# Kernel optimization log

Measured on AMD Instinct MI355X. Metric: run time of the kernel, lower is better.

## Reference

```python
import jax, jax.numpy as jnp
import numpy as np

EPS = 1e-5  # torch LayerNorm default
NUM_HEADS = 12


def layer_norm(x, g, b):
    m = jnp.mean(x, axis=-1, keepdims=True)
    v = jnp.var(x, axis=-1, keepdims=True)
    return (x - m) * jax.lax.rsqrt(v + EPS) * g + b


def split_heads(x):
    B, N, C = x.shape
    return x.reshape(B, N, NUM_HEADS, C // NUM_HEADS).transpose(0, 2, 1, 3)  # [B,H,N,D]


def merge_heads(x):
    B, H, N, D = x.shape
    return x.transpose(0, 2, 1, 3).reshape(B, N, H * D)


def attn_core(q, k, v, mask):
    # q:[B,H,Nq,D], k/v:[B,H,Nk,D], mask:[B,Nk] float (1=keep)
    d = q.shape[-1]
    scores = jnp.einsum('bhqd,bhkd->bhqk', q, k) * (d ** -0.5)
    scores = scores + (1.0 - mask)[:, None, None, :] * -5.0
    a = jax.nn.softmax(scores, axis=-1)
    return jnp.einsum('bhqk,bhkd->bhqd', a, v)


def setup_inputs() -> dict:
    key = jax.random.key(0)
    B, N, C = 4, 1024, 768
    Hd = C * 4  # mlp hidden = 3072
    ks = jax.random.split(key, 12)
    s = 0.02
    inp = {
        'x': jax.random.normal(ks[0], (B, N, C), jnp.float32),
        'encoder_out': jax.random.normal(ks[1], (B, N, C), jnp.float32),
        'mask': jnp.ones((B, N), jnp.float32),
        'encoder_mask': jnp.ones((B, N), jnp.float32),
        'ln1_g': jnp.ones((C,), jnp.float32), 'ln1_b': jnp.zeros((C,), jnp.float32),
        'qkv_w': jax.random.normal(ks[2], (C, 3 * C), jnp.float32) * s,
        'sa_proj_w': jax.random.normal(ks[3], (C, C), jnp.float32) * s,
        'sa_proj_b': jnp.zeros((C,), jnp.float32),
        'ln2_g': jnp.ones((C,), jnp.float32), 'ln2_b': jnp.zeros((C,), jnp.float32),
        'q_w': jax.random.normal(ks[4], (C, C), jnp.float32) * s,
        'kv_w': jax.random.normal(ks[5], (C, 2 * C), jnp.float32) * s,
        'ca_proj_w': jax.random.normal(ks[6], (C, C), jnp.float32) * s,
        'ca_proj_b': jnp.zeros((C,), jnp.float32),
        'ln3_g': jnp.ones((C,), jnp.float32), 'ln3_b': jnp.zeros((C,), jnp.float32),
        'fc1_w': jax.random.normal(ks[7], (C, Hd), jnp.float32) * s,
        'fc1_b': jnp.zeros((Hd,), jnp.float32),
        'fc2_w': jax.random.normal(ks[8], (Hd, C), jnp.float32) * s,
        'fc2_b': jnp.zeros((C,), jnp.float32),
    }
    return inp


def reference(x, encoder_out, mask, encoder_mask,
              ln1_g, ln1_b, qkv_w, sa_proj_w, sa_proj_b,
              ln2_g, ln2_b, q_w, kv_w, ca_proj_w, ca_proj_b,
              ln3_g, ln3_b, fc1_w, fc1_b, fc2_w, fc2_b):
    B, N, C = x.shape
    D = C // NUM_HEADS
    # --- self attention ---
    h = layer_norm(x, ln1_g, ln1_b)
    qkv = (h @ qkv_w).reshape(B, N, 3, NUM_HEADS, D)
    q = qkv[:, :, 0].transpose(0, 2, 1, 3)
    k = qkv[:, :, 1].transpose(0, 2, 1, 3)
    v = qkv[:, :, 2].transpose(0, 2, 1, 3)
    o = merge_heads(attn_core(q, k, v, mask)) @ sa_proj_w + sa_proj_b
    x = x + o
    # --- cross attention ---
    h = layer_norm(x, ln2_g, ln2_b)
    q = split_heads(h @ q_w)
    Be, Ne, Ce = encoder_out.shape
    kv = (encoder_out @ kv_w).reshape(Be, Ne, 2, NUM_HEADS, D)
    k = kv[:, :, 0].transpose(0, 2, 1, 3)
    v = kv[:, :, 1].transpose(0, 2, 1, 3)
    o = merge_heads(attn_core(q, k, v, encoder_mask)) @ ca_proj_w + ca_proj_b
    x = x + o
    # --- MLP (exact GELU, like torch nn.GELU default) ---
    h = layer_norm(x, ln3_g, ln3_b)
    h = jax.nn.gelu(h @ fc1_w + fc1_b, approximate=False) @ fc2_w + fc2_b
    return x + h
```

## Files before the change

kernel.cpp:

```cpp
#include <hip/hip_runtime.h>

typedef __attribute__((ext_vector_type(8))) __bf16 bf16x8;
typedef __attribute__((ext_vector_type(4))) float f32x4;

__device__ __forceinline__ void gload_lds16(const __bf16* g, __bf16* l) {
    __builtin_amdgcn_global_load_lds(
        (const __attribute__((address_space(1))) void*)g,
        (__attribute__((address_space(3))) void*)l,
        16, 0, 0);
}

template <int N> struct WaitVm;
#define WV(n) template <> struct WaitVm<n> { static __device__ __forceinline__ void run() { \
    asm volatile("s_waitcnt vmcnt(" #n ")" ::: "memory"); } };
WV(0) WV(3) WV(4) WV(6) WV(8) WV(9) WV(12)
#undef WV

__global__ void transpose_f2b(const float* __restrict__ in, __bf16* __restrict__ outp,
                              int R, int Ccols) {
    __shared__ __bf16 tile[32][33];
    int bx = blockIdx.x * 32, by = blockIdx.y * 32;
    int tx = threadIdx.x & 31, ty = threadIdx.x >> 5;
#pragma unroll
    for (int i = ty; i < 32; i += 8)
        tile[i][tx] = (__bf16)in[(size_t)(by + i) * Ccols + bx + tx];
    __syncthreads();
#pragma unroll
    for (int i = ty; i < 32; i += 8)
        outp[(size_t)(bx + i) * R + by + tx] = tile[tx][i];
}

__global__ void cvt_f2b(const float* __restrict__ in, __bf16* __restrict__ outp) {
    int i = blockIdx.x * blockDim.x + threadIdx.x;
    float4 v = ((const float4*)in)[i];
    __bf16 o4[4] = {(__bf16)v.x, (__bf16)v.y, (__bf16)v.z, (__bf16)v.w};
    *(uint2*)(outp + (size_t)i * 4) = *(const uint2*)o4;
}

__global__ __launch_bounds__(256) void ln_kernel(const float* __restrict__ x,
                                                 const float* __restrict__ g,
                                                 const float* __restrict__ b,
                                                 __bf16* __restrict__ o) {
    int row = blockIdx.x, tid = threadIdx.x;
    const float* xr = x + (size_t)row * 768;
    float v0 = xr[tid], v1 = xr[tid + 256], v2 = xr[tid + 512];
    float s = v0 + v1 + v2, s2 = v0 * v0 + v1 * v1 + v2 * v2;
#pragma unroll
    for (int d = 32; d >= 1; d >>= 1) {
        s += __shfl_xor(s, d);
        s2 += __shfl_xor(s2, d);
    }
    __shared__ float red[8];
    int wave = tid >> 6, lane = tid & 63;
    if (!lane) { red[wave] = s; red[4 + wave] = s2; }
    __syncthreads();
    s = red[0] + red[1] + red[2] + red[3];
    s2 = red[4] + red[5] + red[6] + red[7];
    float mean = s * (1.0f / 768.0f);
    float var = s2 * (1.0f / 768.0f) - mean * mean;
    float inv = rsqrtf(var + 1e-5f);
    o[(size_t)row * 768 + tid]       = (__bf16)((v0 - mean) * inv * g[tid]       + b[tid]);
    o[(size_t)row * 768 + tid + 256] = (__bf16)((v1 - mean) * inv * g[tid + 256] + b[tid + 256]);
    o[(size_t)row * 768 + tid + 512] = (__bf16)((v2 - mean) * inv * g[tid + 512] + b[tid + 512]);
}

template <int BIAS, int RESID, int GELU, typename TO>
__global__ __launch_bounds__(256) void reduce_splitk(
    const float* __restrict__ P, TO* __restrict__ C,
    const float* __restrict__ bias, const float* __restrict__ resid,
    int total4, int ncols) {
    int i = blockIdx.x * 256 + threadIdx.x;
    if (i >= total4) return;
    float4 a = ((const float4*)P)[i];
    float4 b = ((const float4*)P)[i + total4];
    float v[4] = {a.x + b.x, a.y + b.y, a.z + b.z, a.w + b.w};
    int col = (i * 4) % ncols;
    if (BIAS) {
        float4 bs = *(const float4*)(bias + col);
        v[0] += bs.x; v[1] += bs.y; v[2] += bs.z; v[3] += bs.w;
    }
    if (GELU)
#pragma unroll
        for (int j = 0; j < 4; ++j) v[j] = 0.5f * v[j] * (1.0f + erff(v[j] * 0.70710678118f));
    if (RESID) {
        float4 r = ((const float4*)resid)[i];
        v[0] += r.x; v[1] += r.y; v[2] += r.z; v[3] += r.w;
    }
    TO o4[4] = {(TO)v[0], (TO)v[1], (TO)v[2], (TO)v[3]};
    *(TO*)(&((TO*)C)[(size_t)i * 4]) = o4[0];
    ((TO*)C)[(size_t)i * 4 + 1] = o4[1];
    ((TO*)C)[(size_t)i * 4 + 2] = o4[2];
    ((TO*)C)[(size_t)i * 4 + 3] = o4[3];
}

template <int BM, int NS, int SPLITK, int BIAS, int RESID, int GELU, typename TO>
__global__ __launch_bounds__(256, 2) void gemm_nt(
    const __bf16* __restrict__ A, int lda,
    const __bf16* __restrict__ Bt, int ldb,
    TO* __restrict__ C, int ldc,
    const float* __restrict__ bias,
    const float* __restrict__ resid,
    int K) {
    __shared__ __bf16 lA[NS][BM * 32];
    __shared__ __bf16 lB[NS][128 * 32];
    constexpr int L = (BM == 128) ? 4 : 3;
    constexpr int WCOLS = 256 / BM;
    constexpr int NF = (BM == 128) ? 4 : 2;
    constexpr int WNSP = (BM == 128) ? 64 : 32;
    const int tid = threadIdx.x;
    const int wave = tid >> 6, lane = tid & 63;
    const int wm = wave / WCOLS, wn = wave % WCOLS;
    const int ln15 = lane & 15, hi = lane >> 4;

    const int lin = blockIdx.x + blockIdx.y * gridDim.x;
    const int nwg = gridDim.x * gridDim.y;
    const int t0 = (lin & 7) * (nwg >> 3) + (lin >> 3);
    const int bn = (t0 % gridDim.x) * 128, bm = (t0 / gridDim.x) * BM;

    if constexpr (SPLITK > 1) {
        const int kz = blockIdx.z;
        K /= SPLITK;
        A += (size_t)kz * K;
        Bt += (size_t)kz * K;
        C += (size_t)kz * 4096 * ldc;
    }

    f32x4 acc[4][NF] = {};

    const int srow = tid >> 2;
    const int scol = (((tid & 3) ^ ((srow >> 1) & 3)) * 8);
    const __bf16* gA0 = A + (size_t)(bm + srow) * lda + scol;
    const __bf16* gA1 = A + (size_t)(bm + 64 + srow) * lda + scol;
    const __bf16* gB0 = Bt + (size_t)(bn + srow) * ldb + scol;
    const __bf16* gB1 = Bt + (size_t)(bn + 64 + srow) * ldb + scol;

    const int rswz = (hi * 8) ^ (((ln15 >> 1) & 3) * 8);
    const int rAoff = (wm * 64 + ln15) * 32 + rswz;
    const int rBoff = (wn * WNSP + ln15) * 32 + rswz;

    auto STAGE = [&](int buf, int k0) {
        gload_lds16(gA0 + k0, lA[buf] + wave * 512);
        if constexpr (BM == 128) gload_lds16(gA1 + k0, lA[buf] + 2048 + wave * 512);
        gload_lds16(gB0 + k0, lB[buf] + wave * 512);
        gload_lds16(gB1 + k0, lB[buf] + 2048 + wave * 512);
    };
    auto COMPUTE = [&](int buf) {
        const __bf16* rA = lA[buf] + rAoff;
        const __bf16* rB = lB[buf] + rBoff;
        bf16x8 af[4], bfr[NF];
#pragma unroll
        for (int m = 0; m < 4; ++m) af[m] = *(const bf16x8*)(rA + m * 512);
#pragma unroll
        for (int n = 0; n < NF; ++n) bfr[n] = *(const bf16x8*)(rB + n * 512);
#pragma unroll
        for (int m = 0; m < 4; ++m)
#pragma unroll
            for (int n = 0; n < NF; ++n)
                acc[m][n] = __builtin_amdgcn_mfma_f32_16x16x32_bf16(af[m], bfr[n], acc[m][n], 0, 0, 0);
    };
    auto inc = [](int b) { return (b + 1 == NS) ? 0 : b + 1; };

    const int nt = K >> 5;
#pragma unroll
    for (int s = 0; s < NS - 1; ++s) STAGE(s, s << 5);
    int sbuf = NS - 1, cbuf = 0;
    for (int t = 0; t <= nt - NS; ++t) {
        STAGE(sbuf, (t + NS - 1) << 5);
        sbuf = inc(sbuf);
        WaitVm<(NS - 1) * L>::run();
        __builtin_amdgcn_s_barrier();
        __builtin_amdgcn_sched_barrier(0);
        COMPUTE(cbuf);
        cbuf = inc(cbuf);
        __builtin_amdgcn_sched_barrier(0);
        __builtin_amdgcn_s_barrier();
    }
    if constexpr (NS >= 4) {
        WaitVm<2 * L>::run();
        __builtin_amdgcn_s_barrier();
        __builtin_amdgcn_sched_barrier(0);
        COMPUTE(cbuf); cbuf = inc(cbuf);
        __builtin_amdgcn_sched_barrier(0);
        __builtin_amdgcn_s_barrier();
    }
    if constexpr (NS >= 3) {
        WaitVm<L>::run();
        __builtin_amdgcn_s_barrier();
        __builtin_amdgcn_sched_barrier(0);
        COMPUTE(cbuf); cbuf = inc(cbuf);
        __builtin_amdgcn_sched_barrier(0);
        __builtin_amdgcn_s_barrier();
    }
    WaitVm<0>::run();
    __builtin_amdgcn_s_barrier();
    __builtin_amdgcn_sched_barrier(0);
    COMPUTE(cbuf);

#pragma unroll
    for (int m = 0; m < 4; ++m)
#pragma unroll
        for (int n = 0; n < NF; ++n)
#pragma unroll
            for (int r = 0; r < 4; ++r) {
                int row = bm + wm * 64 + m * 16 + hi * 4 + r;
                int col = bn + wn * WNSP + n * 16 + ln15;
                float v = acc[m][n][r];
                if (BIAS) v += bias[col];
                if (GELU) v = 0.5f * v * (1.0f + erff(v * 0.70710678118f));
                if (RESID) v += resid[(size_t)row * ldc + col];
                C[(size_t)row * ldc + col] = (TO)v;
            }
}

__global__ __launch_bounds__(256, 2) void attn_kernel(
    const __bf16* __restrict__ Qp, int ldq, int qcol,
    const __bf16* __restrict__ Kp, int ldk, int kcol,
    const __bf16* __restrict__ Vp, int ldv, int vcol,
    const float* __restrict__ mask,
    __bf16* __restrict__ Out) {
    __shared__ __bf16 lK[64 * 64];
    __shared__ __bf16 lV[64 * 64];
    __shared__ __bf16 lP[4][16 * 64];
    const int tid = threadIdx.x, wave = tid >> 6, lane = tid & 63;
    const int lin = blockIdx.x + blockIdx.y * 16;
    const int t0 = (lin & 7) * 96 + (lin >> 3);
    const int qt = t0 & 15, bh = t0 >> 4;
    const int b = bh / 12, h = bh % 12;
    const int ln15 = lane & 15, hi = lane >> 4;

    const __bf16* qrow = Qp + (size_t)(b * 1024 + qt * 64 + wave * 16 + ln15) * ldq + qcol + h * 64;
    bf16x8 qf0 = *(const bf16x8*)(qrow + hi * 8);
    bf16x8 qf1 = *(const bf16x8*)(qrow + 32 + hi * 8);

    float l_part[4] = {0.f, 0.f, 0.f, 0.f};
    f32x4 oacc[4] = {};

    const int skey = tid >> 3;
    const int ssrc = (((tid & 7) ^ (skey & 7)) * 8);
    const __bf16* gK = Kp + (size_t)(b * 1024 + skey) * ldk + kcol + h * 64 + ssrc;
    __bf16* lK0 = lK + wave * 512;
    __bf16* lK1 = lK + 2048 + wave * 512;

    const int vkey = tid & 63;
    const int vdb = wave * 16;
    const __bf16* gV = Vp + (size_t)(b * 1024 + vkey) * ldv + vcol + h * 64 + vdb;

    const int kswz = (lane & 7) * 8;
    const __bf16* rK = lK + ln15 * 64;
    const __bf16* rV = lV + ln15 * 64;
    __bf16* wP = lP[wave];
    const __bf16* rP = lP[wave] + ln15 * 64;

    const float C1 = 0.18033688f;
    for (int kt = 0; kt < 16; ++kt) {
        const size_t tb = (size_t)kt * 64;
        gload_lds16(gK + tb * ldk, lK0);
        gload_lds16(gK + (tb + 32) * ldk, lK1);
        bf16x8 v0 = *(const bf16x8*)(gV + tb * ldv);
        bf16x8 v1 = *(const bf16x8*)(gV + tb * ldv + 8);
#pragma unroll
        for (int j = 0; j < 8; ++j) {
            lV[(vdb + j) * 64 + (vkey ^ (j * 8))] = v0[j];
            lV[(vdb + 8 + j) * 64 + (vkey ^ (j * 8))] = v1[j];
        }
        __syncthreads();

        f32x4 s[4];
#pragma unroll
        for (int n = 0; n < 4; ++n) {
            bf16x8 kf0 = *(const bf16x8*)(rK + n * 1024 + ((hi * 8) ^ kswz));
            bf16x8 kf1 = *(const bf16x8*)(rK + n * 1024 + ((hi * 8 + 32) ^ kswz));
            f32x4 z = {};
            z = __builtin_amdgcn_mfma_f32_16x16x32_bf16(qf0, kf0, z, 0, 0, 0);
            s[n] = __builtin_amdgcn_mfma_f32_16x16x32_bf16(qf1, kf1, z, 0, 0, 0);
        }
        float mb2[4];
#pragma unroll
        for (int n = 0; n < 4; ++n)
            mb2[n] = (1.0f - mask[b * 1024 + kt * 64 + n * 16 + ln15]) * -7.2134752f;

#pragma unroll
        for (int n = 0; n < 4; ++n)
#pragma unroll
            for (int r = 0; r < 4; ++r) {
                s[n][r] = exp2f(s[n][r] * C1 + mb2[n]);
                l_part[r] += s[n][r];
            }

#pragma unroll
        for (int n = 0; n < 4; ++n)
#pragma unroll
            for (int r = 0; r < 4; ++r) {
                int prow = hi * 4 + r;
                wP[prow * 64 + ((n * 16 + ln15) ^ ((prow & 7) * 8))] = (__bf16)s[n][r];
            }
        bf16x8 pf0 = *(const bf16x8*)(rP + ((hi * 8) ^ kswz));
        bf16x8 pf1 = *(const bf16x8*)(rP + ((hi * 8 + 32) ^ kswz));
#pragma unroll
        for (int n = 0; n < 4; ++n) {
            bf16x8 vf0 = *(const bf16x8*)(rV + n * 1024 + ((hi * 8) ^ kswz));
            bf16x8 vf1 = *(const bf16x8*)(rV + n * 1024 + ((hi * 8 + 32) ^ kswz));
            oacc[n] = __builtin_amdgcn_mfma_f32_16x16x32_bf16(pf0, vf0, oacc[n], 0, 0, 0);
            oacc[n] = __builtin_amdgcn_mfma_f32_16x16x32_bf16(pf1, vf1, oacc[n], 0, 0, 0);
        }
        __syncthreads();
    }

#pragma unroll
    for (int r = 0; r < 4; ++r) {
#pragma unroll
        for (int d = 1; d < 16; d <<= 1) l_part[r] += __shfl_xor(l_part[r], d);
        l_part[r] = 1.0f / l_part[r];
    }

#pragma unroll
    for (int n = 0; n < 4; ++n)
#pragma unroll
        for (int r = 0; r < 4; ++r) {
            int row = b * 1024 + qt * 64 + wave * 16 + hi * 4 + r;
            int col = h * 64 + n * 16 + ln15;
            Out[(size_t)row * 768 + col] = (__bf16)(oacc[n][r] * l_part[r]);
        }
}

extern "C" void kernel_launch(void* const* d_in, const int* in_sizes, int n_in,
                              void* d_out, int out_size, void* d_ws, size_t ws_size,
                              hipStream_t stream) {
    const float* x     = (const float*)d_in[0];
    const float* enc   = (const float*)d_in[1];
    const float* mask  = (const float*)d_in[2];
    const float* emask = (const float*)d_in[3];
    const float* ln1_g = (const float*)d_in[4];
    const float* ln1_b = (const float*)d_in[5];
    const float* qkv_w = (const float*)d_in[6];
    const float* sa_w  = (const float*)d_in[7];
    const float* sa_b  = (const float*)d_in[8];
    const float* ln2_g = (const float*)d_in[9];
    const float* ln2_b = (const float*)d_in[10];
    const float* q_w   = (const float*)d_in[11];
    const float* kv_w  = (const float*)d_in[12];
    const float* ca_w  = (const float*)d_in[13];
    const float* ca_b  = (const float*)d_in[14];
    const float* ln3_g = (const float*)d_in[15];
    const float* ln3_b = (const float*)d_in[16];
    const float* fc1_w = (const float*)d_in[17];
    const float* fc1_b = (const float*)d_in[18];
    const float* fc2_w = (const float*)d_in[19];
    const float* fc2_b = (const float*)d_in[20];
    float* out = (float*)d_out;

    char* w = (char*)d_ws;
    size_t off = 0;
    auto alloc = [&](size_t bytes) { void* p = w + off; off += bytes; return p; };
    __bf16* qkv_t = (__bf16*)alloc((size_t)2304 * 768 * 2);
    __bf16* sa_t  = (__bf16*)alloc((size_t)768 * 768 * 2);
    __bf16* q_t   = (__bf16*)alloc((size_t)768 * 768 * 2);
    __bf16* kv_t  = (__bf16*)alloc((size_t)1536 * 768 * 2);
    __bf16* ca_t  = (__bf16*)alloc((size_t)768 * 768 * 2);
    __bf16* fc1_t = (__bf16*)alloc((size_t)3072 * 768 * 2);
    __bf16* fc2_t = (__bf16*)alloc((size_t)768 * 3072 * 2);
    __bf16* H     = (__bf16*)alloc((size_t)4096 * 768 * 2);
    __bf16* QKV   = (__bf16*)alloc((size_t)4096 * 2304 * 2);
    __bf16* ATT   = (__bf16*)alloc((size_t)4096 * 768 * 2);
    float*  X1    = (float*)alloc((size_t)4096 * 768 * 4);
    float*  X2    = (float*)alloc((size_t)4096 * 768 * 4);
    __bf16* encb  = (__bf16*)alloc((size_t)4096 * 768 * 2);
    float*  PK    = (float*)alloc((size_t)2 * 4096 * 768 * 4);
    __bf16* HID   = QKV;
    __bf16* Qb    = QKV;
    __bf16* KVb   = QKV + (size_t)4096 * 768;

    dim3 blk(256);
    transpose_f2b<<<dim3(72, 24), blk, 0, stream>>>(qkv_w, qkv_t, 768, 2304);
    transpose_f2b<<<dim3(24, 24), blk, 0, stream>>>(sa_w, sa_t, 768, 768);
    transpose_f2b<<<dim3(24, 24), blk, 0, stream>>>(q_w, q_t, 768, 768);
    transpose_f2b<<<dim3(48, 24), blk, 0, stream>>>(kv_w, kv_t, 768, 1536);
    transpose_f2b<<<dim3(24, 24), blk, 0, stream>>>(ca_w, ca_t, 768, 768);
    transpose_f2b<<<dim3(96, 24), blk, 0, stream>>>(fc1_w, fc1_t, 768, 3072);
    transpose_f2b<<<dim3(24, 96), blk, 0, stream>>>(fc2_w, fc2_t, 3072, 768);
    cvt_f2b<<<dim3(3072), blk, 0, stream>>>(enc, encb);

    ln_kernel<<<4096, blk, 0, stream>>>(x, ln1_g, ln1_b, H);
    gemm_nt<128, 3, 1, 0, 0, 0, __bf16><<<dim3(18, 32), blk, 0, stream>>>(H, 768, qkv_t, 768, QKV, 2304, nullptr, nullptr, 768);
    attn_kernel<<<dim3(16, 48), blk, 0, stream>>>(QKV, 2304, 0, QKV, 2304, 768, QKV, 2304, 1536, mask, ATT);
    gemm_nt<64, 4, 1, 1, 1, 0, float><<<dim3(6, 64), blk, 0, stream>>>(ATT, 768, sa_t, 768, X1, 768, sa_b, x, 768);
    ln_kernel<<<4096, blk, 0, stream>>>(X1, ln2_g, ln2_b, H);
    gemm_nt<64, 4, 1, 0, 0, 0, __bf16><<<dim3(6, 64), blk, 0, stream>>>(H, 768, q_t, 768, Qb, 768, nullptr, nullptr, 768);
    gemm_nt<128, 3, 1, 0, 0, 0, __bf16><<<dim3(12, 32), blk, 0, stream>>>(encb, 768, kv_t, 768, KVb, 1536, nullptr, nullptr, 768);
    attn_kernel<<<dim3(16, 48), blk, 0, stream>>>(Qb, 768, 0, KVb, 1536, 0, KVb, 1536, 768, emask, ATT);
    gemm_nt<64, 4, 1, 1, 1, 0, float><<<dim3(6, 64), blk, 0, stream>>>(ATT, 768, ca_t, 768, X2, 768, ca_b, X1, 768);
    ln_kernel<<<4096, blk, 0, stream>>>(X2, ln3_g, ln3_b, H);
    gemm_nt<128, 3, 1, 1, 0, 1, __bf16><<<dim3(24, 32), blk, 0, stream>>>(H, 768, fc1_t, 768, HID, 3072, fc1_b, nullptr, 768);
    gemm_nt<64, 4, 2, 0, 0, 0, float><<<dim3(6, 64, 2), blk, 0, stream>>>(HID, 3072, fc2_t, 3072, PK, 768, nullptr, nullptr, 3072);
    reduce_splitk<1, 1, 0, float><<<dim3(3072), blk, 0, stream>>>(PK, out, fc2_b, X2, 786432, 768);
}
```

Measured before the change: 418.7 us.

## Merge weight prep into one launch, use polynomial GELU, retile fc1 GEMM

```diff
diff --git a/kernel.cpp b/kernel.cpp
--- a/kernel.cpp
+++ b/kernel.cpp
@@ -16,25 +16,52 @@
 WV(0) WV(3) WV(4) WV(6) WV(8) WV(9) WV(12)
 #undef WV
 
-__global__ void transpose_f2b(const float* __restrict__ in, __bf16* __restrict__ outp,
-                              int R, int Ccols) {
+__device__ __forceinline__ float gelu_f(float x) {
+    float z = fabsf(x) * 0.70710678118f;
+    float t = 1.0f / (1.0f + 0.3275911f * z);
+    float poly = t * (0.254829592f + t * (-0.284496736f +
+                 t * (1.421413741f + t * (-1.453152027f + t * 1.061405429f))));
+    float erfv = 1.0f - poly * __expf(-z * z);
+    erfv = (x < 0.f) ? -erfv : erfv;
+    return 0.5f * x * (1.0f + erfv);
+}
+
+__global__ __launch_bounds__(256) void prep_all(
+    const float* __restrict__ qkv_w, __bf16* __restrict__ qkv_t,
+    const float* __restrict__ sa_w,  __bf16* __restrict__ sa_t,
+    const float* __restrict__ q_w,   __bf16* __restrict__ q_t,
+    const float* __restrict__ kv_w,  __bf16* __restrict__ kv_t,
+    const float* __restrict__ ca_w,  __bf16* __restrict__ ca_t,
+    const float* __restrict__ fc1_w, __bf16* __restrict__ fc1_t,
+    const float* __restrict__ fc2_w, __bf16* __restrict__ fc2_t,
+    const float* __restrict__ enc,   __bf16* __restrict__ encb) {
     __shared__ __bf16 tile[32][33];
-    int bx = blockIdx.x * 32, by = blockIdx.y * 32;
-    int tx = threadIdx.x & 31, ty = threadIdx.x >> 5;
+    const int b = blockIdx.x;
+    const float* in; __bf16* out; int R, C, l;
+    if (b < 1728)      { in = qkv_w; out = qkv_t; R = 768;  C = 2304; l = b; }
+    else if (b < 2304) { in = sa_w;  out = sa_t;  R = 768;  C = 768;  l = b - 1728; }
+    else if (b < 2880) { in = q_w;   out = q_t;   R = 768;  C = 768;  l = b - 2304; }
+    else if (b < 4032) { in = kv_w;  out = kv_t;  R = 768;  C = 1536; l = b - 2880; }
+    else if (b < 4608) { in = ca_w;  out = ca_t;  R = 768;  C = 768;  l = b - 4032; }
+    else if (b < 6912) { in = fc1_w; out = fc1_t; R = 768;  C = 3072; l = b - 4608; }
+    else if (b < 9216) { in = fc2_w; out = fc2_t; R = 3072; C = 768;  l = b - 6912; }
+    else {
+        int i = (b - 9216) * 256 + threadIdx.x;
+        float4 v = ((const float4*)enc)[i];
+        __bf16 o4[4] = {(__bf16)v.x, (__bf16)v.y, (__bf16)v.z, (__bf16)v.w};
+        *(uint2*)(encb + (size_t)i * 4) = *(const uint2*)o4;
+        return;
+    }
+    const int txn = C >> 5;
+    const int bx = (l % txn) << 5, by = (l / txn) << 5;
+    const int tx = threadIdx.x & 31, ty = threadIdx.x >> 5;
 #pragma unroll
     for (int i = ty; i < 32; i += 8)
-        tile[i][tx] = (__bf16)in[(size_t)(by + i) * Ccols + bx + tx];
+        tile[i][tx] = (__bf16)in[(size_t)(by + i) * C + bx + tx];
     __syncthreads();
 #pragma unroll
     for (int i = ty; i < 32; i += 8)
-        outp[(size_t)(bx + i) * R + by + tx] = tile[tx][i];
-}
-
-__global__ void cvt_f2b(const float* __restrict__ in, __bf16* __restrict__ outp) {
-    int i = blockIdx.x * blockDim.x + threadIdx.x;
-    float4 v = ((const float4*)in)[i];
-    __bf16 o4[4] = {(__bf16)v.x, (__bf16)v.y, (__bf16)v.z, (__bf16)v.w};
-    *(uint2*)(outp + (size_t)i * 4) = *(const uint2*)o4;
+        out[(size_t)(bx + i) * R + by + tx] = tile[tx][i];
 }
 
 __global__ __launch_bounds__(256) void ln_kernel(const float* __restrict__ x,
@@ -81,19 +108,18 @@
     }
     if (GELU)
 #pragma unroll
-        for (int j = 0; j < 4; ++j) v[j] = 0.5f * v[j] * (1.0f + erff(v[j] * 0.70710678118f));
+        for (int j = 0; j < 4; ++j) v[j] = gelu_f(v[j]);
     if (RESID) {
         float4 r = ((const float4*)resid)[i];
         v[0] += r.x; v[1] += r.y; v[2] += r.z; v[3] += r.w;
     }
-    TO o4[4] = {(TO)v[0], (TO)v[1], (TO)v[2], (TO)v[3]};
-    *(TO*)(&((TO*)C)[(size_t)i * 4]) = o4[0];
-    ((TO*)C)[(size_t)i * 4 + 1] = o4[1];
-    ((TO*)C)[(size_t)i * 4 + 2] = o4[2];
-    ((TO*)C)[(size_t)i * 4 + 3] = o4[3];
-}
-
-template <int BM, int NS, int SPLITK, int BIAS, int RESID, int GELU, typename TO>
+    ((TO*)C)[(size_t)i * 4]     = (TO)v[0];
+    ((TO*)C)[(size_t)i * 4 + 1] = (TO)v[1];
+    ((TO*)C)[(size_t)i * 4 + 2] = (TO)v[2];
+    ((TO*)C)[(size_t)i * 4 + 3] = (TO)v[3];
+}
+
+template <int BM, int NS, int SPLITK, int BIAS, int RESID, int GELU, int SWZ, typename TO>
 __global__ __launch_bounds__(256, 2) void gemm_nt(
     const __bf16* __restrict__ A, int lda,
     const __bf16* __restrict__ Bt, int ldb,
@@ -112,10 +138,15 @@
     const int wm = wave / WCOLS, wn = wave % WCOLS;
     const int ln15 = lane & 15, hi = lane >> 4;
 
-    const int lin = blockIdx.x + blockIdx.y * gridDim.x;
-    const int nwg = gridDim.x * gridDim.y;
-    const int t0 = (lin & 7) * (nwg >> 3) + (lin >> 3);
-    const int bn = (t0 % gridDim.x) * 128, bm = (t0 / gridDim.x) * BM;
+    int bn, bm;
+    if constexpr (SWZ) {
+        const int lin = blockIdx.x + blockIdx.y * gridDim.x;
+        const int nwg = gridDim.x * gridDim.y;
+        const int t0 = (lin & 7) * (nwg >> 3) + (lin >> 3);
+        bn = (t0 % gridDim.x) * 128; bm = (t0 / gridDim.x) * BM;
+    } else {
+        bn = blockIdx.x * 128; bm = blockIdx.y * BM;
+    }
 
     if constexpr (SPLITK > 1) {
         const int kz = blockIdx.z;
@@ -206,7 +237,7 @@
                 int col = bn + wn * WNSP + n * 16 + ln15;
                 float v = acc[m][n][r];
                 if (BIAS) v += bias[col];
-                if (GELU) v = 0.5f * v * (1.0f + erff(v * 0.70710678118f));
+                if (GELU) v = gelu_f(v);
                 if (RESID) v += resid[(size_t)row * ldc + col];
                 C[(size_t)row * ldc + col] = (TO)v;
             }
@@ -371,26 +402,21 @@
     __bf16* KVb   = QKV + (size_t)4096 * 768;
 
     dim3 blk(256);
-    transpose_f2b<<<dim3(72, 24), blk, 0, stream>>>(qkv_w, qkv_t, 768, 2304);
-    transpose_f2b<<<dim3(24, 24), blk, 0, stream>>>(sa_w, sa_t, 768, 768);
-    transpose_f2b<<<dim3(24, 24), blk, 0, stream>>>(q_w, q_t, 768, 768);
-    transpose_f2b<<<dim3(48, 24), blk, 0, stream>>>(kv_w, kv_t, 768, 1536);
-    transpose_f2b<<<dim3(24, 24), blk, 0, stream>>>(ca_w, ca_t, 768, 768);
-    transpose_f2b<<<dim3(96, 24), blk, 0, stream>>>(fc1_w, fc1_t, 768, 3072);
-    transpose_f2b<<<dim3(24, 96), blk, 0, stream>>>(fc2_w, fc2_t, 3072, 768);
-    cvt_f2b<<<dim3(3072), blk, 0, stream>>>(enc, encb);
+    prep_all<<<dim3(12288), blk, 0, stream>>>(qkv_w, qkv_t, sa_w, sa_t, q_w, q_t,
+                                              kv_w, kv_t, ca_w, ca_t, fc1_w, fc1_t,
+                                              fc2_w, fc2_t, enc, encb);
 
     ln_kernel<<<4096, blk, 0, stream>>>(x, ln1_g, ln1_b, H);
-    gemm_nt<128, 3, 1, 0, 0, 0, __bf16><<<dim3(18, 32), blk, 0, stream>>>(H, 768, qkv_t, 768, QKV, 2304, nullptr, nullptr, 768);
+    gemm_nt<128, 3, 1, 0, 0, 0, 1, __bf16><<<dim3(18, 32), blk, 0, stream>>>(H, 768, qkv_t, 768, QKV, 2304, nullptr, nullptr, 768);
     attn_kernel<<<dim3(16, 48), blk, 0, stream>>>(QKV, 2304, 0, QKV, 2304, 768, QKV, 2304, 1536, mask, ATT);
-    gemm_nt<64, 4, 1, 1, 1, 0, float><<<dim3(6, 64), blk, 0, stream>>>(ATT, 768, sa_t, 768, X1, 768, sa_b, x, 768);
+    gemm_nt<64, 4, 1, 1, 1, 0, 1, float><<<dim3(6, 64), blk, 0, stream>>>(ATT, 768, sa_t, 768, X1, 768, sa_b, x, 768);
     ln_kernel<<<4096, blk, 0, stream>>>(X1, ln2_g, ln2_b, H);
-    gemm_nt<64, 4, 1, 0, 0, 0, __bf16><<<dim3(6, 64), blk, 0, stream>>>(H, 768, q_t, 768, Qb, 768, nullptr, nullptr, 768);
-    gemm_nt<128, 3, 1, 0, 0, 0, __bf16><<<dim3(12, 32), blk, 0, stream>>>(encb, 768, kv_t, 768, KVb, 1536, nullptr, nullptr, 768);
+    gemm_nt<64, 4, 1, 0, 0, 0, 1, __bf16><<<dim3(6, 64), blk, 0, stream>>>(H, 768, q_t, 768, Qb, 768, nullptr, nullptr, 768);
+    gemm_nt<128, 3, 1, 0, 0, 0, 1, __bf16><<<dim3(12, 32), blk, 0, stream>>>(encb, 768, kv_t, 768, KVb, 1536, nullptr, nullptr, 768);
     attn_kernel<<<dim3(16, 48), blk, 0, stream>>>(Qb, 768, 0, KVb, 1536, 0, KVb, 1536, 768, emask, ATT);
-    gemm_nt<64, 4, 1, 1, 1, 0, float><<<dim3(6, 64), blk, 0, stream>>>(ATT, 768, ca_t, 768, X2, 768, ca_b, X1, 768);
+    gemm_nt<64, 4, 1, 1, 1, 0, 1, float><<<dim3(6, 64), blk, 0, stream>>>(ATT, 768, ca_t, 768, X2, 768, ca_b, X1, 768);
     ln_kernel<<<4096, blk, 0, stream>>>(X2, ln3_g, ln3_b, H);
-    gemm_nt<128, 3, 1, 1, 0, 1, __bf16><<<dim3(24, 32), blk, 0, stream>>>(H, 768, fc1_t, 768, HID, 3072, fc1_b, nullptr, 768);
-    gemm_nt<64, 4, 2, 0, 0, 0, float><<<dim3(6, 64, 2), blk, 0, stream>>>(HID, 3072, fc2_t, 3072, PK, 768, nullptr, nullptr, 3072);
+    gemm_nt<64, 2, 1, 1, 0, 1, 0, __bf16><<<dim3(24, 64), blk, 0, stream>>>(H, 768, fc1_t, 768, HID, 3072, fc1_b, nullptr, 768);
+    gemm_nt<64, 4, 2, 0, 0, 0, 1, float><<<dim3(6, 64, 2), blk, 0, stream>>>(HID, 3072, fc2_t, 3072, PK, 768, nullptr, nullptr, 3072);
     reduce_splitk<1, 1, 0, float><<<dim3(3072), blk, 0, stream>>>(PK, out, fc2_b, X2, 786432, 768);
 }
```

Result: faster. 405.1 us (-3.2%).
